# Kernel tuning notes

Hardware: AMD Instinct MI355X
Metric: run time of the kernel (lower is better)

Reference implementation:

```python
import jax, jax.numpy as jnp
import numpy as np

B, T, N, D = 2, 10, 1024, 1024
NH = 16
HD = D // NH


def setup_inputs() -> dict:
    key = jax.random.key(0)
    ks = jax.random.split(key, 9)
    data = jax.random.normal(ks[0], (B, N, D), jnp.float32)
    traj_pos = jax.random.normal(ks[1], (B, T, N, 3), jnp.float32)
    q = jax.random.normal(ks[2], (B, T, N, 4), jnp.float32)
    traj_quat = q / (jnp.linalg.norm(q, axis=-1, keepdims=True) + 1e-10)
    certainty = jax.random.uniform(ks[3], (B, N), jnp.float32)
    s = 1.0 / np.sqrt(D).astype(np.float32)
    Wq = jax.random.normal(ks[4], (D, D), jnp.float32) * s
    Wk = jax.random.normal(ks[5], (D, D), jnp.float32) * s
    Wv = jax.random.normal(ks[6], (D, D), jnp.float32) * s
    Wo = jax.random.normal(ks[7], (D, D), jnp.float32) * s
    z = jnp.zeros((D,), jnp.float32)
    return {"data": data, "traj_pos": traj_pos, "traj_quat": traj_quat,
            "certainty": certainty, "Wq": Wq, "bq": z, "Wk": Wk, "bk": z,
            "Wv": Wv, "bv": z, "Wo": Wo, "bo": z}


def reference(data, traj_pos, traj_quat, certainty, Wq, bq, Wk, bk, Wv, bv, Wo, bo):
    b, n, d = data.shape
    # --- trajectory similarity scores (same for all batches: torch.mean over batch+time) ---
    # pos_dist[i,j] = mean_{b,t} ||p_bti - p_btj||
    pd = jnp.linalg.norm(traj_pos[:, :, :, None, :] - traj_pos[:, :, None, :, :], axis=-1).mean(axis=(0, 1))  # (n,n)
    qdm = jnp.linalg.norm(traj_quat[:, :, :, None, :] - traj_quat[:, :, None, :, :], axis=-1).mean(axis=(0, 1))
    qdp = jnp.linalg.norm(traj_quat[:, :, :, None, :] + traj_quat[:, :, None, :, :], axis=-1).mean(axis=(0, 1))
    qd = jnp.minimum(qdm, qdp)
    traj = jnp.exp(-pd - qd)
    traj = traj / traj.sum(axis=-1, keepdims=True)  # (n,n) row-normalized

    def proj(x, W, bias):
        return (x @ W.T + bias).reshape(b, n, NH, HD).transpose(0, 2, 1, 3)  # (b,h,n,hd)

    Q = proj(data, Wq, bq)
    K = proj(data, Wk, bk)
    V = proj(data, Wv, bv)
    scores = jnp.einsum('bhid,bhjd->bhij', Q, K) / np.sqrt(HD).astype(np.float32)
    combined = scores + 0.5 * traj[None, None]  # broadcast over (batch, heads)
    attn = jax.nn.softmax(combined, axis=-1)
    out = jnp.einsum('bhij,bhjd->bhid', attn, V).transpose(0, 2, 1, 3).reshape(b, n, d)
    out = out @ Wo.T + bo
    # certainty update from attention entropy
    avg_attn = attn.mean(axis=1)  # (b,n,n)
    p = jnp.clip(avg_attn, 1e-10, None)
    Hent = -jnp.sum(p * jnp.log(p), axis=-1)  # (b,n)
    H_max = np.log(n).astype(np.float32)
    new_certainty = jnp.maximum(certainty, jax.nn.sigmoid(H_max - Hent))
    return out, new_certainty
```

## Files before the change

kernel.cpp:

```cpp
#include <hip/hip_runtime.h>
#include <math.h>

#define NB 2
#define NN 1024
#define DD 1024
#define NHH 16
#define HDD 64
#define BTT 20

typedef unsigned short u16;
typedef short bf16x8 __attribute__((ext_vector_type(8)));
typedef float f32x4 __attribute__((ext_vector_type(4)));

#define HMAXL 6.93147180559945f
#define C1 0.18033688011112042f
#define TLC 0.72134752044448170f
#define KC  0.072134752044448170f
#define CH 520

#define TRAJ_OFF 0
#define TL_OFF    1048576
#define DATAB_OFF 1572864
#define WQB_OFF   2621440
#define WKB_OFF   3145728
#define WVB_OFF   3670016
#define WOB_OFF   4194304
#define QB_OFF    4718592
#define KB_OFF    5767168
#define VT_OFF    6815744
#define AOB_OFF   7864320
#define LV_OFF    8912896
#define HPART_OFF 8945664
#define RSP_OFF   8978432

__device__ __forceinline__ float b2f(u16 h) { return __uint_as_float(((unsigned)h) << 16); }
__device__ __forceinline__ u16 f2bf(float f) {
  unsigned u = __float_as_uint(f);
  return (u16)((u + 0x7fffu + ((u >> 16) & 1u)) >> 16);
}
__device__ __forceinline__ void dma16(const void* g, void* l) {
  __builtin_amdgcn_global_load_lds((const __attribute__((address_space(1))) void*)g,
                                   (__attribute__((address_space(3))) void*)l, 16, 0, 0);
}

__global__ __launch_bounds__(256) void conv_kernel(const float* __restrict__ data,
                                                   const float* __restrict__ w0,
                                                   const float* __restrict__ w1,
                                                   const float* __restrict__ w2,
                                                   const float* __restrict__ w3,
                                                   u16* __restrict__ dd,
                                                   u16* __restrict__ d0, u16* __restrict__ d1,
                                                   u16* __restrict__ d2, u16* __restrict__ d3) {
  int z = blockIdx.y;
  const float* s;
  u16* d;
  size_t off = 0;
  if (z < 2) { s = data; d = dd; off = (size_t)z * 1048576; }
  else if (z == 2) { s = w0; d = d0; }
  else if (z == 3) { s = w1; d = d1; }
  else if (z == 4) { s = w2; d = d2; }
  else { s = w3; d = d3; }
  size_t i = off + (size_t)(blockIdx.x * 256 + threadIdx.x) * 4;
  float4 v = *(const float4*)(s + i);
  ushort4 o = {f2bf(v.x), f2bf(v.y), f2bf(v.z), f2bf(v.w)};
  *(ushort4*)(d + i) = o;
}

__global__ __launch_bounds__(256) void trajA_kernel(const float* __restrict__ pos,
                                                    const float* __restrict__ quat,
                                                    float* __restrict__ w,
                                                    float* __restrict__ rsp) {
  const int tid = threadIdx.x;
  const int jx = blockIdx.x;
  const int j = jx * 256 + tid;
  const int i0 = blockIdx.y * 8;
  __shared__ float ld[8][BTT][8];
  __shared__ float wredS[4][8];
  if (tid < 8 * BTT) {
    int ii = tid / BTT, bt = tid % BTT;
    const float* pp = pos + ((size_t)bt * NN + i0 + ii) * 3;
    ld[ii][bt][0] = pp[0]; ld[ii][bt][1] = pp[1]; ld[ii][bt][2] = pp[2];
    *(float4*)&ld[ii][bt][4] = *(const float4*)(quat + ((size_t)bt * NN + i0 + ii) * 4);
  }
  __syncthreads();
  float acc[8] = {};
  for (int bt = 0; bt < BTT; ++bt) {
    const float* pj = pos + ((size_t)bt * NN + j) * 3;
    float pjx = pj[0], pjy = pj[1], pjz = pj[2];
    float4 qj = *(const float4*)(quat + ((size_t)bt * NN + j) * 4);
#pragma unroll
    for (int ii = 0; ii < 8; ++ii) {
      float4 pi = *(const float4*)&ld[ii][bt][0];
      float4 qi = *(const float4*)&ld[ii][bt][4];
      float dx = pi.x - pjx, dy = pi.y - pjy, dz = pi.z - pjz;
      float d2 = fmaf(dz, dz, fmaf(dy, dy, dx * dx));
      float dot = fmaf(qi.w, qj.w, fmaf(qi.z, qj.z, fmaf(qi.y, qj.y, qi.x * qj.x)));
      float tq = fmaf(-2.f, fabsf(dot), 2.f);
      acc[ii] += sqrtf(d2) + sqrtf(fmaxf(tq, 0.f));
    }
  }
  const int wv = tid >> 6;
#pragma unroll
  for (int ii = 0; ii < 8; ++ii) {
    float v = exp2f(-acc[ii] * KC);
    w[(size_t)(i0 + ii) * NN + j] = v;
    float s = v;
#pragma unroll
    for (int off = 1; off < 64; off <<= 1) s += __shfl_xor(s, off, 64);
    if ((tid & 63) == 0) wredS[wv][ii] = s;
  }
  __syncthreads();
  if (tid < 8)
    rsp[jx * 1024 + i0 + tid] = wredS[0][tid] + wredS[1][tid] + wredS[2][tid] + wredS[3][tid];
}

__global__ __launch_bounds__(256) void qkv_trajB_kernel(const u16* __restrict__ Ab,
                                                        const u16* __restrict__ Wq,
                                                        const u16* __restrict__ Wk,
                                                        const u16* __restrict__ Wv,
                                                        const float* __restrict__ bq,
                                                        const float* __restrict__ bk,
                                                        const float* __restrict__ bv,
                                                        u16* __restrict__ Qb,
                                                        u16* __restrict__ Kb,
                                                        u16* __restrict__ VtT,
                                                        const float* __restrict__ wtr,
                                                        const float* __restrict__ rsp,
                                                        u16* __restrict__ tl) {
  const int tid = threadIdx.x;
  __shared__ __align__(16) u16 As[128 * 32];
  __shared__ __align__(16) u16 Bs[128 * 32];
  if (blockIdx.x < 256) {
    int base = blockIdx.x * 4;
#pragma unroll
    for (int r = 0; r < 4; ++r) {
      int i = base + r;
      float inv = TLC / (rsp[i] + rsp[1024 + i] + rsp[2048 + i] + rsp[3072 + i]);
      float4 w4 = *(const float4*)(wtr + (size_t)i * NN + tid * 4);
      ushort4 o = {f2bf(w4.x * inv), f2bf(w4.y * inv), f2bf(w4.z * inv), f2bf(w4.w * inv)};
      *(ushort4*)(tl + (size_t)i * NN + tid * 4) = o;
    }
    return;
  }
  const int bid = blockIdx.x - 256;
  const int z = bid >> 7;
  const int rem = bid & 127;
  const int bxg = rem & 7, byg = rem >> 3;
  const u16* Wb = z == 0 ? Wq : (z == 1 ? Wk : Wv);
  const float* bias = z == 0 ? bq : (z == 1 ? bk : bv);
  const int w = tid >> 6, l = tid & 63, g = l >> 4, ln = l & 15;
  const int bm = byg << 7, bn = bxg << 7;
  const int srow = w * 16 + (l >> 2);
  const int scol = (l & 3) * 8;
  const u16* Ap0 = Ab + (size_t)(bm + srow) * DD + scol;
  const u16* Ap1 = Ab + (size_t)(bm + 64 + srow) * DD + scol;
  const u16* Bp0 = Wb + (size_t)(bn + srow) * DD + scol;
  const u16* Bp1 = Wb + (size_t)(bn + 64 + srow) * DD + scol;
  u16* dA0 = As + w * 512;
  u16* dA1 = As + 2048 + w * 512;
  u16* dB0 = Bs + w * 512;
  u16* dB1 = Bs + 2048 + w * 512;
  const int mw = (w & 1) * 64, nw = (w >> 1) * 64;
  f32x4 zero4 = {0.f, 0.f, 0.f, 0.f};
  f32x4 acc[4][4];
#pragma unroll
  for (int mt = 0; mt < 4; ++mt)
#pragma unroll
    for (int nt = 0; nt < 4; ++nt) acc[mt][nt] = zero4;
  for (int k0 = 0; k0 < DD; k0 += 32) {
    __syncthreads();
    dma16(Ap0 + k0, dA0); dma16(Ap1 + k0, dA1);
    dma16(Bp0 + k0, dB0); dma16(Bp1 + k0, dB1);
    __syncthreads();
    bf16x8 bfr[4], afr[4];
#pragma unroll
    for (int nt = 0; nt < 4; ++nt)
      bfr[nt] = *(const bf16x8*)&Bs[(nw + nt * 16 + ln) * 32 + g * 8];
#pragma unroll
    for (int mt = 0; mt < 4; ++mt)
      afr[mt] = *(const bf16x8*)&As[(mw + mt * 16 + ln) * 32 + g * 8];
#pragma unroll
    for (int mt = 0; mt < 4; ++mt)
#pragma unroll
      for (int nt = 0; nt < 4; ++nt)
        acc[mt][nt] = __builtin_amdgcn_mfma_f32_16x16x32_bf16(afr[mt], bfr[nt], acc[mt][nt], 0, 0, 0);
  }
#pragma unroll
  for (int nt = 0; nt < 4; ++nt) {
    int n = bn + nw + nt * 16 + ln;
    float bb = bias[n];
    if (z == 2) {
      int row = (((bm >> 10) << 4) + (n >> 6)) * 64 + (n & 63);
#pragma unroll
      for (int mt = 0; mt < 4; ++mt) {
        int tok = (bm & 1023) + mw + mt * 16 + g * 4;
        ushort4 pk = {f2bf(acc[mt][nt][0] + bb), f2bf(acc[mt][nt][1] + bb),
                      f2bf(acc[mt][nt][2] + bb), f2bf(acc[mt][nt][3] + bb)};
        *(ushort4*)(VtT + (size_t)row * NN + tok) = pk;
      }
    } else {
      u16* outp = z == 0 ? Qb : Kb;
#pragma unroll
      for (int mt = 0; mt < 4; ++mt) {
#pragma unroll
        for (int r = 0; r < 4; ++r) {
          int m = bm + mw + mt * 16 + g * 4 + r;
          outp[(size_t)m * DD + n] = f2bf(acc[mt][nt][r] + bb);
        }
      }
    }
  }
}

__global__ __launch_bounds__(256) void att_kernel(const u16* __restrict__ Qb,
                                                  const u16* __restrict__ Kb,
                                                  const u16* __restrict__ VtT,
                                                  const u16* __restrict__ tl,
                                                  u16* __restrict__ AOb,
                                                  float* __restrict__ Lv) {
  const int tid = threadIdx.x;
  const int bh = blockIdx.y;
  const int b = bh >> 4, h = bh & 15;
  const int i0 = blockIdx.x << 6;
  const int w = tid >> 6, l = tid & 63, g = l >> 4, ln = l & 15;
  const int wi0 = w * 16;
  __shared__ __align__(16) u16 Qs[8 * CH];
  __shared__ __align__(16) u16 Ks[2][8 * CH];
  __shared__ __align__(16) u16 Vts[2][8 * CH];
  __shared__ __align__(16) u16 Pt[64 * 72];
  __shared__ float lsc[64];
  const int c0 = 2 * w, c1 = 2 * w + 1;
  const int rr = 8 * (l >> 3);
  const int dcol = (l & 7) * 8;
  dma16(Qb + ((size_t)(b * NN) + i0 + c0 + rr) * DD + h * HDD + dcol, Qs + c0 * CH);
  dma16(Qb + ((size_t)(b * NN) + i0 + c1 + rr) * DD + h * HDD + dcol, Qs + c1 * CH);
  const int ig = i0 + wi0 + ln;
  const int lnlo = (ln & 7) * CH;
  const int lnhi = (ln >> 3) * 64;
  f32x4 zero4 = {0.f, 0.f, 0.f, 0.f};
  f32x4 oacc[4];
#pragma unroll
  for (int nt = 0; nt < 4; ++nt) oacc[nt] = zero4;
  float lacc = 0.f;
  for (int j0 = 0; j0 < NN; j0 += 128) {
    __syncthreads();
#pragma unroll
    for (int u = 0; u < 2; ++u) {
      int jb = j0 + u * 64;
      dma16(Kb + ((size_t)(b * NN) + jb + c0 + rr) * DD + h * HDD + dcol, Ks[u] + c0 * CH);
      dma16(Kb + ((size_t)(b * NN) + jb + c1 + rr) * DD + h * HDD + dcol, Ks[u] + c1 * CH);
      dma16(VtT + ((size_t)(bh * 64) + c0 + rr) * NN + jb + dcol, Vts[u] + c0 * CH);
      dma16(VtT + ((size_t)(bh * 64) + c1 + rr) * NN + jb + dcol, Vts[u] + c1 * CH);
    }
    ushort4 tlv[2][4];
#pragma unroll
    for (int u = 0; u < 2; ++u)
#pragma unroll
      for (int jt = 0; jt < 4; ++jt)
        tlv[u][jt] = *(const ushort4*)(tl + (size_t)ig * NN + j0 + u * 64 + jt * 16 + g * 4);
    __syncthreads();
    bf16x8 qf[2];
    qf[0] = *(const bf16x8*)&Qs[lnlo + (2 * w) * 64 + lnhi + g * 8];
    qf[1] = *(const bf16x8*)&Qs[lnlo + (2 * w) * 64 + lnhi + 32 + g * 8];
#pragma unroll
    for (int u = 0; u < 2; ++u) {
      f32x4 sacc[4];
#pragma unroll
      for (int jt = 0; jt < 4; ++jt) {
        sacc[jt] = zero4;
#pragma unroll
        for (int kc = 0; kc < 2; ++kc) {
          bf16x8 af = *(const bf16x8*)&Ks[u][lnlo + (2 * jt) * 64 + lnhi + kc * 32 + g * 8];
          sacc[jt] = __builtin_amdgcn_mfma_f32_16x16x32_bf16(af, qf[kc], sacc[jt], 0, 0, 0);
        }
      }
#pragma unroll
      for (int jt = 0; jt < 4; ++jt) {
        float e0 = exp2f(sacc[jt][0] * C1 + b2f(tlv[u][jt].x));
        float e1 = exp2f(sacc[jt][1] * C1 + b2f(tlv[u][jt].y));
        float e2 = exp2f(sacc[jt][2] * C1 + b2f(tlv[u][jt].z));
        float e3 = exp2f(sacc[jt][3] * C1 + b2f(tlv[u][jt].w));
        lacc += (e0 + e1) + (e2 + e3);
        ushort4 pk = {f2bf(e0), f2bf(e1), f2bf(e2), f2bf(e3)};
        *(ushort4*)(Pt + (wi0 + ln) * 72 + jt * 16 + g * 4) = pk;
      }
      bf16x8 pf[2];
      pf[0] = *(const bf16x8*)&Pt[(wi0 + ln) * 72 + g * 8];
      pf[1] = *(const bf16x8*)&Pt[(wi0 + ln) * 72 + 32 + g * 8];
#pragma unroll
      for (int nt = 0; nt < 4; ++nt) {
#pragma unroll
        for (int kc = 0; kc < 2; ++kc) {
          bf16x8 vf = *(const bf16x8*)&Vts[u][lnlo + (2 * nt) * 64 + lnhi + kc * 32 + g * 8];
          oacc[nt] = __builtin_amdgcn_mfma_f32_16x16x32_bf16(pf[kc], vf, oacc[nt], 0, 0, 0);
        }
      }
    }
  }
  lacc += __shfl_xor(lacc, 16, 64);
  lacc += __shfl_xor(lacc, 32, 64);
  if (g == 0) {
    Lv[(size_t)bh * NN + i0 + wi0 + ln] = lacc;
    lsc[wi0 + ln] = 1.f / lacc;
  }
  __syncthreads();
#pragma unroll
  for (int nt = 0; nt < 4; ++nt) {
    int d = nt * 16 + ln;
#pragma unroll
    for (int r = 0; r < 4; ++r) {
      int i = wi0 + g * 4 + r;
      float v = oacc[nt][r] * lsc[i];
      AOb[((size_t)(b * NN) + i0 + i) * DD + h * HDD + d] = f2bf(v);
    }
  }
}

__global__ __launch_bounds__(256) void ent_kernel(const u16* __restrict__ Qb,
                                                  const u16* __restrict__ Kb,
                                                  const u16* __restrict__ tl,
                                                  const float* __restrict__ Lv,
                                                  float* __restrict__ Hp) {
  const int tid = threadIdx.x;
  const int jx = blockIdx.x & 15;
  const int iy = (blockIdx.x >> 4) & 15;
  const int b = blockIdx.x >> 8;
  const int j0 = jx << 6, i0 = iy << 6;
  const int w = tid >> 6, l = tid & 63, g = l >> 4, ln = l & 15;
  const int wi0 = w * 16;
  __shared__ __align__(16) u16 Qs[32 * CH];
  __shared__ __align__(16) u16 Ks[32 * CH];
  __shared__ float linv[NHH * 64];
#pragma unroll
  for (int rep = 0; rep < 4; ++rep) {
    int idx = tid + (rep << 8);
    int hh = idx >> 6, ii = idx & 63;
    linv[hh * 64 + ii] = 1.f / Lv[((size_t)((b << 4) + hh)) * NN + i0 + ii];
  }
  const int rlo = l >> 5;
  const int scol = (l & 31) * 8;
  const int ig = i0 + wi0 + ln;
  const int elo = (ln >> 1) * CH;
  const int ehi = (ln & 1) * 256;
  ushort4 tlv[4];
#pragma unroll
  for (int jt = 0; jt < 4; ++jt)
    tlv[jt] = *(const ushort4*)(tl + (size_t)ig * NN + j0 + jt * 16 + g * 4);
  float P[4][4] = {};
  f32x4 zero4 = {0.f, 0.f, 0.f, 0.f};
  for (int hb = 0; hb < 4; ++hb) {
    __syncthreads();
#pragma unroll
    for (int cc = 0; cc < 8; ++cc) {
      int c = w * 8 + cc;
      dma16(Qb + ((size_t)(b * NN) + i0 + 2 * c + rlo) * DD + hb * 256 + scol, Qs + c * CH);
      dma16(Kb + ((size_t)(b * NN) + j0 + 2 * c + rlo) * DD + hb * 256 + scol, Ks + c * CH);
    }
    __syncthreads();
#pragma unroll
    for (int hl = 0; hl < 4; ++hl) {
      float li = linv[(hb * 4 + hl) * 64 + wi0 + ln];
      bf16x8 qf[2];
      qf[0] = *(const bf16x8*)&Qs[(w * 8) * CH + elo + ehi + hl * 64 + g * 8];
      qf[1] = *(const bf16x8*)&Qs[(w * 8) * CH + elo + ehi + hl * 64 + 32 + g * 8];
#pragma unroll
      for (int jt = 0; jt < 4; ++jt) {
        f32x4 sacc = zero4;
#pragma unroll
        for (int kc = 0; kc < 2; ++kc) {
          bf16x8 af = *(const bf16x8*)&Ks[(jt * 8) * CH + elo + ehi + hl * 64 + kc * 32 + g * 8];
          sacc = __builtin_amdgcn_mfma_f32_16x16x32_bf16(af, qf[kc], sacc, 0, 0, 0);
        }
        P[jt][0] += exp2f(sacc[0] * C1 + b2f(tlv[jt].x)) * li;
        P[jt][1] += exp2f(sacc[1] * C1 + b2f(tlv[jt].y)) * li;
        P[jt][2] += exp2f(sacc[2] * C1 + b2f(tlv[jt].z)) * li;
        P[jt][3] += exp2f(sacc[3] * C1 + b2f(tlv[jt].w)) * li;
      }
    }
  }
  float hs = 0.f;
#pragma unroll
  for (int jt = 0; jt < 4; ++jt) {
#pragma unroll
    for (int r = 0; r < 4; ++r) {
      float p = fmaxf(P[jt][r] * (1.f / NHH), 1e-10f);
      hs -= p * logf(p);
    }
  }
  hs += __shfl_xor(hs, 16, 64);
  hs += __shfl_xor(hs, 32, 64);
  if (g == 0) Hp[jx * 2048 + (size_t)b * NN + i0 + wi0 + ln] = hs;
}

__global__ __launch_bounds__(256) void gemmo_cert_kernel(const u16* __restrict__ Ab,
                                                         const u16* __restrict__ Wb,
                                                         const float* __restrict__ bias,
                                                         float* __restrict__ C,
                                                         const float* __restrict__ Hp,
                                                         const float* __restrict__ cert,
                                                         float* __restrict__ outc) {
  const int tid = threadIdx.x;
  __shared__ __align__(16) u16 As[128 * 32];
  __shared__ __align__(16) u16 Bs[128 * 32];
  if (blockIdx.x >= 128) {
    int idx = (blockIdx.x - 128) * 256 + tid;
    float H = 0.f;
#pragma unroll
    for (int jt = 0; jt < 16; ++jt) H += Hp[jt * 2048 + idx];
    float sg = 1.f / (1.f + expf(H - HMAXL));
    outc[idx] = fmaxf(cert[idx], sg);
    return;
  }
  const int bxg = blockIdx.x & 7, byg = blockIdx.x >> 3;
  const int w = tid >> 6, l = tid & 63, g = l >> 4, ln = l & 15;
  const int bm = byg << 7, bn = bxg << 7;
  const int srow = w * 16 + (l >> 2);
  const int scol = (l & 3) * 8;
  const u16* Ap0 = Ab + (size_t)(bm + srow) * DD + scol;
  const u16* Ap1 = Ab + (size_t)(bm + 64 + srow) * DD + scol;
  const u16* Bp0 = Wb + (size_t)(bn + srow) * DD + scol;
  const u16* Bp1 = Wb + (size_t)(bn + 64 + srow) * DD + scol;
  u16* dA0 = As + w * 512;
  u16* dA1 = As + 2048 + w * 512;
  u16* dB0 = Bs + w * 512;
  u16* dB1 = Bs + 2048 + w * 512;
  const int mw = (w & 1) * 64, nw = (w >> 1) * 64;
  f32x4 zero4 = {0.f, 0.f, 0.f, 0.f};
  f32x4 acc[4][4];
#pragma unroll
  for (int mt = 0; mt < 4; ++mt)
#pragma unroll
    for (int nt = 0; nt < 4; ++nt) acc[mt][nt] = zero4;
  for (int k0 = 0; k0 < DD; k0 += 32) {
    __syncthreads();
    dma16(Ap0 + k0, dA0); dma16(Ap1 + k0, dA1);
    dma16(Bp0 + k0, dB0); dma16(Bp1 + k0, dB1);
    __syncthreads();
    bf16x8 bfr[4], afr[4];
#pragma unroll
    for (int nt = 0; nt < 4; ++nt)
      bfr[nt] = *(const bf16x8*)&Bs[(nw + nt * 16 + ln) * 32 + g * 8];
#pragma unroll
    for (int mt = 0; mt < 4; ++mt)
      afr[mt] = *(const bf16x8*)&As[(mw + mt * 16 + ln) * 32 + g * 8];
#pragma unroll
    for (int mt = 0; mt < 4; ++mt)
#pragma unroll
      for (int nt = 0; nt < 4; ++nt)
        acc[mt][nt] = __builtin_amdgcn_mfma_f32_16x16x32_bf16(afr[mt], bfr[nt], acc[mt][nt], 0, 0, 0);
  }
#pragma unroll
  for (int nt = 0; nt < 4; ++nt) {
    int n = bn + nw + nt * 16 + ln;
    float bb = bias[n];
#pragma unroll
    for (int mt = 0; mt < 4; ++mt) {
#pragma unroll
      for (int r = 0; r < 4; ++r) {
        int m = bm + mw + mt * 16 + g * 4 + r;
        C[(size_t)m * DD + n] = acc[mt][nt][r] + bb;
      }
    }
  }
}

extern "C" void kernel_launch(void* const* d_in, const int* in_sizes, int n_in,
                              void* d_out, int out_size, void* d_ws, size_t ws_size,
                              hipStream_t stream) {
  const float* data      = (const float*)d_in[0];
  const float* traj_pos  = (const float*)d_in[1];
  const float* traj_quat = (const float*)d_in[2];
  const float* certainty = (const float*)d_in[3];
  const float* Wq = (const float*)d_in[4];
  const float* bq = (const float*)d_in[5];
  const float* Wk = (const float*)d_in[6];
  const float* bk = (const float*)d_in[7];
  const float* Wv = (const float*)d_in[8];
  const float* bv = (const float*)d_in[9];
  const float* Wo = (const float*)d_in[10];
  const float* bo = (const float*)d_in[11];

  float* ws = (float*)d_ws;
  float* wtr  = ws + TRAJ_OFF;
  u16* tl    = (u16*)(ws + TL_OFF);
  u16* datab = (u16*)(ws + DATAB_OFF);
  u16* wqb   = (u16*)(ws + WQB_OFF);
  u16* wkb   = (u16*)(ws + WKB_OFF);
  u16* wvb   = (u16*)(ws + WVB_OFF);
  u16* wob   = (u16*)(ws + WOB_OFF);
  u16* Qb    = (u16*)(ws + QB_OFF);
  u16* Kb    = (u16*)(ws + KB_OFF);
  u16* VtT   = (u16*)(ws + VT_OFF);
  u16* AOb   = (u16*)(ws + AOB_OFF);
  float* Lv   = ws + LV_OFF;
  float* Hp   = ws + HPART_OFF;
  float* rsp  = ws + RSP_OFF;
  float* out  = (float*)d_out;
  float* outc = out + (size_t)NB * NN * DD;

  conv_kernel<<<dim3(1024, 6), 256, 0, stream>>>(data, Wq, Wk, Wv, Wo,
                                                 datab, wqb, wkb, wvb, wob);
  trajA_kernel<<<dim3(4, 128), 256, 0, stream>>>(traj_pos, traj_quat, wtr, rsp);
  qkv_trajB_kernel<<<640, 256, 0, stream>>>(datab, wqb, wkb, wvb, bq, bk, bv,
                                            Qb, Kb, VtT, wtr, rsp, tl);
  att_kernel<<<dim3(NN / 64, NB * NHH), 256, 0, stream>>>(Qb, Kb, VtT, tl, AOb, Lv);
  ent_kernel<<<512, 256, 0, stream>>>(Qb, Kb, tl, Lv, Hp);
  gemmo_cert_kernel<<<136, 256, 0, stream>>>(AOb, wob, bo, out, Hp, certainty, outc);
}
```

Measured before the change: 223.7 us.

## Merge conv and trajA launches, add MFMA setprio, shrink output GEMM tile

```diff
diff --git a/kernel.cpp b/kernel.cpp
--- a/kernel.cpp
+++ b/kernel.cpp
@@ -43,39 +43,42 @@
                                    (__attribute__((address_space(3))) void*)l, 16, 0, 0);
 }
 
-__global__ __launch_bounds__(256) void conv_kernel(const float* __restrict__ data,
+__global__ __launch_bounds__(256) void prep_kernel(const float* __restrict__ data,
                                                    const float* __restrict__ w0,
                                                    const float* __restrict__ w1,
                                                    const float* __restrict__ w2,
                                                    const float* __restrict__ w3,
                                                    u16* __restrict__ dd,
                                                    u16* __restrict__ d0, u16* __restrict__ d1,
-                                                   u16* __restrict__ d2, u16* __restrict__ d3) {
-  int z = blockIdx.y;
-  const float* s;
-  u16* d;
-  size_t off = 0;
-  if (z < 2) { s = data; d = dd; off = (size_t)z * 1048576; }
-  else if (z == 2) { s = w0; d = d0; }
-  else if (z == 3) { s = w1; d = d1; }
-  else if (z == 4) { s = w2; d = d2; }
-  else { s = w3; d = d3; }
-  size_t i = off + (size_t)(blockIdx.x * 256 + threadIdx.x) * 4;
-  float4 v = *(const float4*)(s + i);
-  ushort4 o = {f2bf(v.x), f2bf(v.y), f2bf(v.z), f2bf(v.w)};
-  *(ushort4*)(d + i) = o;
-}
-
-__global__ __launch_bounds__(256) void trajA_kernel(const float* __restrict__ pos,
-                                                    const float* __restrict__ quat,
-                                                    float* __restrict__ w,
-                                                    float* __restrict__ rsp) {
+                                                   u16* __restrict__ d2, u16* __restrict__ d3,
+                                                   const float* __restrict__ pos,
+                                                   const float* __restrict__ quat,
+                                                   float* __restrict__ w,
+                                                   float* __restrict__ rsp) {
   const int tid = threadIdx.x;
-  const int jx = blockIdx.x;
-  const int j = jx * 256 + tid;
-  const int i0 = blockIdx.y * 8;
+  const int bid = blockIdx.x;
   __shared__ float ld[8][BTT][8];
   __shared__ float wredS[4][8];
+  if (bid >= 512) {
+    int cb = bid - 512;
+    int z = cb >> 10;
+    const float* s;
+    u16* d;
+    size_t off = 0;
+    if (z < 2) { s = data; d = dd; off = (size_t)z * 1048576; }
+    else if (z == 2) { s = w0; d = d0; }
+    else if (z == 3) { s = w1; d = d1; }
+    else if (z == 4) { s = w2; d = d2; }
+    else { s = w3; d = d3; }
+    size_t i = off + (size_t)((cb & 1023) * 256 + tid) * 4;
+    float4 v = *(const float4*)(s + i);
+    ushort4 o = {f2bf(v.x), f2bf(v.y), f2bf(v.z), f2bf(v.w)};
+    *(ushort4*)(d + i) = o;
+    return;
+  }
+  const int jx = bid & 3;
+  const int j = jx * 256 + tid;
+  const int i0 = (bid >> 2) * 8;
   if (tid < 8 * BTT) {
     int ii = tid / BTT, bt = tid % BTT;
     const float* pp = pos + ((size_t)bt * NN + i0 + ii) * 3;
@@ -265,6 +268,7 @@
 #pragma unroll
     for (int u = 0; u < 2; ++u) {
       f32x4 sacc[4];
+      __builtin_amdgcn_s_setprio(1);
 #pragma unroll
       for (int jt = 0; jt < 4; ++jt) {
         sacc[jt] = zero4;
@@ -274,6 +278,7 @@
           sacc[jt] = __builtin_amdgcn_mfma_f32_16x16x32_bf16(af, qf[kc], sacc[jt], 0, 0, 0);
         }
       }
+      __builtin_amdgcn_s_setprio(0);
 #pragma unroll
       for (int jt = 0; jt < 4; ++jt) {
         float e0 = exp2f(sacc[jt][0] * C1 + b2f(tlv[u][jt].x));
@@ -287,6 +292,7 @@
       bf16x8 pf[2];
       pf[0] = *(const bf16x8*)&Pt[(wi0 + ln) * 72 + g * 8];
       pf[1] = *(const bf16x8*)&Pt[(wi0 + ln) * 72 + 32 + g * 8];
+      __builtin_amdgcn_s_setprio(1);
 #pragma unroll
       for (int nt = 0; nt < 4; ++nt) {
 #pragma unroll
@@ -295,6 +301,7 @@
           oacc[nt] = __builtin_amdgcn_mfma_f32_16x16x32_bf16(pf[kc], vf, oacc[nt], 0, 0, 0);
         }
       }
+      __builtin_amdgcn_s_setprio(0);
     }
   }
   lacc += __shfl_xor(lacc, 16, 64);
@@ -366,11 +373,13 @@
 #pragma unroll
       for (int jt = 0; jt < 4; ++jt) {
         f32x4 sacc = zero4;
+        __builtin_amdgcn_s_setprio(1);
 #pragma unroll
         for (int kc = 0; kc < 2; ++kc) {
           bf16x8 af = *(const bf16x8*)&Ks[(jt * 8) * CH + elo + ehi + hl * 64 + kc * 32 + g * 8];
           sacc = __builtin_amdgcn_mfma_f32_16x16x32_bf16(af, qf[kc], sacc, 0, 0, 0);
         }
+        __builtin_amdgcn_s_setprio(0);
         P[jt][0] += exp2f(sacc[0] * C1 + b2f(tlv[jt].x)) * li;
         P[jt][1] += exp2f(sacc[1] * C1 + b2f(tlv[jt].y)) * li;
         P[jt][2] += exp2f(sacc[2] * C1 + b2f(tlv[jt].z)) * li;
@@ -401,9 +410,9 @@
                                                          float* __restrict__ outc) {
   const int tid = threadIdx.x;
   __shared__ __align__(16) u16 As[128 * 32];
-  __shared__ __align__(16) u16 Bs[128 * 32];
-  if (blockIdx.x >= 128) {
-    int idx = (blockIdx.x - 128) * 256 + tid;
+  __shared__ __align__(16) u16 Bs[64 * 32];
+  if (blockIdx.x >= 256) {
+    int idx = (blockIdx.x - 256) * 256 + tid;
     float H = 0.f;
 #pragma unroll
     for (int jt = 0; jt < 16; ++jt) H += Hp[jt * 2048 + idx];
@@ -411,34 +420,32 @@
     outc[idx] = fmaxf(cert[idx], sg);
     return;
   }
-  const int bxg = blockIdx.x & 7, byg = blockIdx.x >> 3;
+  const int bn = (blockIdx.x & 15) << 6;
+  const int bm = (blockIdx.x >> 4) << 7;
   const int w = tid >> 6, l = tid & 63, g = l >> 4, ln = l & 15;
-  const int bm = byg << 7, bn = bxg << 7;
   const int srow = w * 16 + (l >> 2);
   const int scol = (l & 3) * 8;
   const u16* Ap0 = Ab + (size_t)(bm + srow) * DD + scol;
   const u16* Ap1 = Ab + (size_t)(bm + 64 + srow) * DD + scol;
   const u16* Bp0 = Wb + (size_t)(bn + srow) * DD + scol;
-  const u16* Bp1 = Wb + (size_t)(bn + 64 + srow) * DD + scol;
   u16* dA0 = As + w * 512;
   u16* dA1 = As + 2048 + w * 512;
   u16* dB0 = Bs + w * 512;
-  u16* dB1 = Bs + 2048 + w * 512;
-  const int mw = (w & 1) * 64, nw = (w >> 1) * 64;
+  const int mw = (w & 1) * 64, nw = (w >> 1) * 32;
   f32x4 zero4 = {0.f, 0.f, 0.f, 0.f};
-  f32x4 acc[4][4];
+  f32x4 acc[4][2];
 #pragma unroll
   for (int mt = 0; mt < 4; ++mt)
 #pragma unroll
-    for (int nt = 0; nt < 4; ++nt) acc[mt][nt] = zero4;
+    for (int nt = 0; nt < 2; ++nt) acc[mt][nt] = zero4;
   for (int k0 = 0; k0 < DD; k0 += 32) {
     __syncthreads();
     dma16(Ap0 + k0, dA0); dma16(Ap1 + k0, dA1);
-    dma16(Bp0 + k0, dB0); dma16(Bp1 + k0, dB1);
-    __syncthreads();
-    bf16x8 bfr[4], afr[4];
-#pragma unroll
-    for (int nt = 0; nt < 4; ++nt)
+    dma16(Bp0 + k0, dB0);
+    __syncthreads();
+    bf16x8 bfr[2], afr[4];
+#pragma unroll
+    for (int nt = 0; nt < 2; ++nt)
       bfr[nt] = *(const bf16x8*)&Bs[(nw + nt * 16 + ln) * 32 + g * 8];
 #pragma unroll
     for (int mt = 0; mt < 4; ++mt)
@@ -446,11 +453,11 @@
 #pragma unroll
     for (int mt = 0; mt < 4; ++mt)
 #pragma unroll
-      for (int nt = 0; nt < 4; ++nt)
+      for (int nt = 0; nt < 2; ++nt)
         acc[mt][nt] = __builtin_amdgcn_mfma_f32_16x16x32_bf16(afr[mt], bfr[nt], acc[mt][nt], 0, 0, 0);
   }
 #pragma unroll
-  for (int nt = 0; nt < 4; ++nt) {
+  for (int nt = 0; nt < 2; ++nt) {
     int n = bn + nw + nt * 16 + ln;
     float bb = bias[n];
 #pragma unroll
@@ -498,12 +505,12 @@
   float* out  = (float*)d_out;
   float* outc = out + (size_t)NB * NN * DD;
 
-  conv_kernel<<<dim3(1024, 6), 256, 0, stream>>>(data, Wq, Wk, Wv, Wo,
-                                                 datab, wqb, wkb, wvb, wob);
-  trajA_kernel<<<dim3(4, 128), 256, 0, stream>>>(traj_pos, traj_quat, wtr, rsp);
+  prep_kernel<<<6656, 256, 0, stream>>>(data, Wq, Wk, Wv, Wo,
+                                        datab, wqb, wkb, wvb, wob,
+                                        traj_pos, traj_quat, wtr, rsp);
   qkv_trajB_kernel<<<640, 256, 0, stream>>>(datab, wqb, wkb, wvb, bq, bk, bv,
                                             Qb, Kb, VtT, wtr, rsp, tl);
   att_kernel<<<dim3(NN / 64, NB * NHH), 256, 0, stream>>>(Qb, Kb, VtT, tl, AOb, Lv);
   ent_kernel<<<512, 256, 0, stream>>>(Qb, Kb, tl, Lv, Hp);
-  gemmo_cert_kernel<<<136, 256, 0, stream>>>(AOb, wob, bo, out, Hp, certainty, outc);
-}
+  gemmo_cert_kernel<<<264, 256, 0, stream>>>(AOb, wob, bo, out, Hp, certainty, outc);
+}
```

After: 208.3 us. 1.07x faster.
